# Performance work log

Hardware: AMD Instinct MI355X
Metric: run time of the kernel (lower is better)

Reference implementation:

```python
import jax, jax.numpy as jnp
import numpy as np

B, S, D, H, DH = 2, 2048, 256, 8, 32
INNER = H * DH


def setup_inputs() -> dict:
    key = jax.random.key(0)
    ks = jax.random.split(key, 8)
    x = jax.random.normal(ks[0], (B, S, D), dtype=jnp.float32)
    mask = jax.random.randint(ks[1], (B, S), 0, 2) > 0  # bool, ~half valid
    attn_bias = jax.random.normal(ks[2], (B, H, S, S), dtype=jnp.float32) * 0.1
    Wq = jax.random.normal(ks[3], (D, INNER), dtype=jnp.float32) * 0.02
    Wkv = jax.random.normal(ks[4], (D, 2 * INNER), dtype=jnp.float32) * 0.02
    Wo = jax.random.normal(ks[5], (INNER, D), dtype=jnp.float32) * 0.02
    bo = jnp.zeros((D,), dtype=jnp.float32)
    Wg = jax.random.normal(ks[6], (D, INNER), dtype=jnp.float32) * 0.02
    bg = jnp.ones((INNER,), dtype=jnp.float32)  # torch init: gating bias = 1.0
    return {"x": x, "mask": mask, "attn_bias": attn_bias, "Wq": Wq,
            "Wkv": Wkv, "Wo": Wo, "bo": bo, "Wg": Wg, "bg": bg}


def reference(x, mask, attn_bias, Wq, Wkv, Wo, bo, Wg, bg):
    scale = DH ** -0.5
    b, s, _ = x.shape
    # q,k,v projections; '... i (h d) -> ... h i d'
    q = (x @ Wq).reshape(b, s, H, DH).swapaxes(1, 2)            # [b,h,s,d]
    kv = x @ Wkv
    k, v = jnp.split(kv, 2, axis=-1)
    k = k.reshape(b, s, H, DH).swapaxes(1, 2)                   # [b,h,s,d]
    v = v.reshape(b, s, H, DH).swapaxes(1, 2)                   # [b,h,s,d]
    # scores with additive bias and boolean masking
    dots = jnp.einsum('bhid,bhjd->bhij', q * scale, k) + attn_bias
    amask = mask[:, None, :, None] & mask[:, None, None, :]     # [b,1,i,j]
    neg = -jnp.finfo(dots.dtype).max
    dots = jnp.where(amask, dots, neg)
    attn = jax.nn.softmax(dots, axis=-1)                        # dropout p=0 (eval)
    out = jnp.einsum('bhij,bhjd->bhid', attn, v)
    out = out.swapaxes(1, 2).reshape(b, s, INNER)               # '... h i d -> ... i (h d)'
    gates = jax.nn.sigmoid(x @ Wg + bg)
    out = out * gates
    return out @ Wo + bo
```

## Files before the change

### kernel.cpp

```cpp
#include <hip/hip_runtime.h>
#include <float.h>

typedef unsigned short u16;
typedef __attribute__((ext_vector_type(8))) short bf16x8;
typedef __attribute__((ext_vector_type(4))) float f32x4;

#define LOG2E 1.4426950408889634f
#define B_ 2
#define S_ 2048
#define D_ 256
#define H_ 8
#define DH_ 32
#define M_ 4096

__device__ __forceinline__ void gload_lds16(const void* g, void* l) {
  __builtin_amdgcn_global_load_lds(
      (const __attribute__((address_space(1))) unsigned int*)g,
      (__attribute__((address_space(3))) unsigned int*)l, 16, 0, 0);
}

__device__ __forceinline__ u16 f2bf(float f) {
  unsigned u = __float_as_uint(f);
  unsigned r = (u + 0x7FFFu + ((u >> 16) & 1u)) >> 16;
  return (u16)r;
}

__global__ __launch_bounds__(256) void conv_x(const float* __restrict__ x,
                                              u16* __restrict__ xb) {
  int i = (blockIdx.x * 256 + threadIdx.x) * 4;
  float4 v = *(const float4*)(x + i);
  ushort4 o;
  o.x = f2bf(v.x); o.y = f2bf(v.y); o.z = f2bf(v.z); o.w = f2bf(v.w);
  *(ushort4*)(xb + i) = o;
}

__global__ __launch_bounds__(256) void prep_w(const float* __restrict__ Wq,
                                              const float* __restrict__ Wkv,
                                              const float* __restrict__ Wo,
                                              const float* __restrict__ Wg,
                                              u16* __restrict__ wt,
                                              u16* __restrict__ wot) {
  int t = blockIdx.x * 256 + threadIdx.x;
  const float scale = 0.17677669529663687f;
  if (t < 65536) {
    int k = t >> 8, n = t & 255;
    wt[(size_t)n * 256 + k] = f2bf(Wq[t] * scale);
  } else if (t < 196608) {
    int s = t - 65536;
    int k = s >> 9, c = s & 511;
    int n = (c < 256) ? (256 + c) : (512 + (c - 256));
    wt[(size_t)n * 256 + k] = f2bf(Wkv[s]);
  } else if (t < 262144) {
    int s = t - 196608;
    int k = s >> 8, n = s & 255;
    wt[(size_t)(768 + n) * 256 + k] = f2bf(Wg[s]);
  } else {
    int s = t - 262144;
    int k = s >> 8, n = s & 255;
    wot[(size_t)n * 256 + k] = f2bf(Wo[s]);
  }
}

__global__ __launch_bounds__(64) void pack_mask(const int* __restrict__ mask,
                                                unsigned* __restrict__ cmT) {
  int b = blockIdx.x, c = threadIdx.x;
  unsigned wd = 0;
#pragma unroll
  for (int jc = 0; jc < 32; ++jc)
    wd |= (unsigned)(mask[b * 2048 + jc * 64 + c] & 1) << jc;
  cmT[b * 64 + c] = wd;
}

__global__ __launch_bounds__(256) void gemm_proj(
    const u16* __restrict__ xb, const u16* __restrict__ wt,
    const float* __restrict__ bg, u16* __restrict__ qs, u16* __restrict__ kb,
    u16* __restrict__ vt, float* __restrict__ gates) {
  __shared__ u16 lA[2][128 * 32];
  __shared__ u16 lB[2][128 * 32];
  const int tid = threadIdx.x, l = tid & 63, w = tid >> 6;
  const int m0 = blockIdx.x * 128, n0 = blockIdx.y * 128;
  const int wm = w >> 1, wn = w & 1;
  f32x4 acc[4][4];
#pragma unroll
  for (int i = 0; i < 4; ++i)
#pragma unroll
    for (int j = 0; j < 4; ++j) acc[i][j] = (f32x4){0.f, 0.f, 0.f, 0.f};

  auto stage = [&](int ks, int p) {
#pragma unroll
    for (int i = 0; i < 2; ++i) {
      int slot = i * 256 + tid;
      int row = slot >> 2, sk = slot & 3;
      int sw = sk ^ ((row >> 1) & 3);
      gload_lds16(xb + (size_t)(m0 + row) * 256 + ks * 32 + sw * 8,
                  (char*)lA[p] + slot * 16);
    }
#pragma unroll
    for (int i = 0; i < 2; ++i) {
      int slot = i * 256 + tid;
      int row = slot >> 2, sk = slot & 3;
      int sw = sk ^ ((row >> 1) & 3);
      gload_lds16(wt + (size_t)(n0 + row) * 256 + ks * 32 + sw * 8,
                  (char*)lB[p] + slot * 16);
    }
  };

  stage(0, 0);
  asm volatile("s_waitcnt vmcnt(0)" ::: "memory");
  __builtin_amdgcn_s_barrier();

  for (int ks = 0; ks < 8; ++ks) {
    const int cur = ks & 1;
    if (ks < 7) {
      stage(ks + 1, cur ^ 1);
      asm volatile("s_waitcnt vmcnt(4)" ::: "memory");
    } else {
      asm volatile("s_waitcnt vmcnt(0)" ::: "memory");
    }
    __builtin_amdgcn_s_barrier();

    bf16x8 af[4], bfr[4];
#pragma unroll
    for (int mi = 0; mi < 4; ++mi) {
      int row = wm * 64 + mi * 16 + (l & 15);
      int koff = ((l >> 4) << 4) ^ (((row >> 1) & 3) << 4);
      af[mi] = *(const bf16x8*)((const char*)lA[cur] + row * 64 + koff);
    }
#pragma unroll
    for (int ni = 0; ni < 4; ++ni) {
      int row = wn * 64 + ni * 16 + (l & 15);
      int koff = ((l >> 4) << 4) ^ (((row >> 1) & 3) << 4);
      bfr[ni] = *(const bf16x8*)((const char*)lB[cur] + row * 64 + koff);
    }
#pragma unroll
    for (int mi = 0; mi < 4; ++mi)
#pragma unroll
      for (int ni = 0; ni < 4; ++ni)
        acc[mi][ni] = __builtin_amdgcn_mfma_f32_16x16x32_bf16(
            af[mi], bfr[ni], acc[mi][ni], 0, 0, 0);
    __builtin_amdgcn_sched_barrier(0);
    __builtin_amdgcn_s_barrier();
  }
  const int region = n0 >> 8;
#pragma unroll
  for (int mi = 0; mi < 4; ++mi)
#pragma unroll
    for (int ni = 0; ni < 4; ++ni) {
      int row = m0 + wm * 64 + mi * 16 + ((l >> 4) << 2);
      int col = n0 + wn * 64 + ni * 16 + (l & 15);
      int c = col & 255;
#pragma unroll
      for (int r = 0; r < 4; ++r) {
        float v = acc[mi][ni][r];
        int rr = row + r;
        int bq = rr >> 11, s = rr & 2047;
        if (region == 0) {
          int h = c >> 5, dh = c & 31;
          qs[((((size_t)bq * 8 + h) * 2048 + s) << 5) + dh] = f2bf(v);
        } else if (region == 1) {
          int h = c >> 5, dh = c & 31;
          kb[((((size_t)bq * 8 + h) * 2048 + s) << 5) + dh] = f2bf(v);
        } else if (region == 2) {
          int h = c >> 5, dh = c & 31;
          vt[((((size_t)bq * 8 + h) * 32 + dh) << 11) + s] = f2bf(v);
        } else {
          float g = 1.f / (1.f + expf(-(v + bg[c])));
          gates[(size_t)rr * 256 + c] = g;
        }
      }
    }
}

__global__ __launch_bounds__(256) void attn_fwd(
    const u16* __restrict__ qs, const u16* __restrict__ kb,
    const u16* __restrict__ vt, const float* __restrict__ bias,
    const int* __restrict__ mask, const unsigned* __restrict__ cmT,
    const float* __restrict__ gates, u16* __restrict__ ao) {
  __shared__ u16 lK[2][64 * 32];
  __shared__ u16 lV[2][32 * 64];
  __shared__ float lBias[2][64 * 64];
  __shared__ u16 lP[4][16 * 64];
  const int tid = threadIdx.x, l = tid & 63, w = tid >> 6;
  const int qt = blockIdx.x, h = blockIdx.y, b = blockIdx.z;
  const int q0 = qt * 64;
  const size_t bh = (size_t)b * H_ + h;

  const int qrow = q0 + w * 16 + (l & 15);
  bf16x8 qf = *(const bf16x8*)(qs + ((bh * S_ + qrow) << 5) + ((l >> 4) << 3));

  int rowr[4], mi_[4];
  float m_i[4], l_i[4];
  unsigned cm[4];
  f32x4 acc_o[2];
  acc_o[0] = (f32x4){0.f, 0.f, 0.f, 0.f};
  acc_o[1] = (f32x4){0.f, 0.f, 0.f, 0.f};
#pragma unroll
  for (int r = 0; r < 4; ++r) {
    rowr[r] = q0 + w * 16 + ((l >> 4) << 2) + r;
    mi_[r] = mask[b * S_ + rowr[r]] & 1;
    m_i[r] = -FLT_MAX;
    l_i[r] = 0.f;
  }
#pragma unroll
  for (int cg = 0; cg < 4; ++cg) cm[cg] = cmT[(b << 6) + cg * 16 + (l & 15)];

  auto stage = [&](int jc, int p) {
    const int j0 = jc * 64;
    {
      int row = tid >> 2, sk = tid & 3;
      int sw = sk ^ ((row >> 1) & 3);
      gload_lds16(kb + ((bh * S_ + j0 + row) << 5) + sw * 8,
                  (char*)lK[p] + tid * 16);
    }
    {
      int dh = tid >> 3, sk = tid & 7;
      int sw = sk ^ (dh & 7);
      gload_lds16(vt + ((bh * 32 + dh) << 11) + j0 + sw * 8,
                  (char*)lV[p] + tid * 16);
    }
#pragma unroll
    for (int i = 0; i < 4; ++i) {
      int u = i * 256 + tid;
      int row = u >> 4, cb = u & 15;
      gload_lds16(bias + (bh * S_ + q0 + row) * (size_t)S_ + j0 + cb * 4,
                  (char*)lBias[p] + u * 16);
    }
  };

  stage(0, 0);
  asm volatile("s_waitcnt vmcnt(0)" ::: "memory");
  __builtin_amdgcn_s_barrier();

  for (int jc = 0; jc < 32; ++jc) {
    const int cur = jc & 1;
    if (jc < 31) {
      stage(jc + 1, cur ^ 1);
      asm volatile("s_waitcnt vmcnt(6)" ::: "memory");
    } else {
      asm volatile("s_waitcnt vmcnt(0)" ::: "memory");
    }
    __builtin_amdgcn_s_barrier();

    f32x4 sc[4];
#pragma unroll
    for (int cg = 0; cg < 4; ++cg) {
      int colj = cg * 16 + (l & 15);
      int mj = (int)((cm[cg] >> jc) & 1u);
      f32x4 ci;
#pragma unroll
      for (int r = 0; r < 4; ++r) {
        int qlr = w * 16 + ((l >> 4) << 2) + r;
        float bv = lBias[cur][qlr * 64 + colj];
        ci[r] = (mi_[r] & mj) ? bv : -FLT_MAX;
      }
      int krow = cg * 16 + (l & 15);
      int koff = ((l >> 4) << 4) ^ (((krow >> 1) & 3) << 4);
      bf16x8 kf = *(const bf16x8*)((const char*)lK[cur] + krow * 64 + koff);
      sc[cg] = __builtin_amdgcn_mfma_f32_16x16x32_bf16(qf, kf, ci, 0, 0, 0);
    }

    float corr[4];
#pragma unroll
    for (int r = 0; r < 4; ++r) {
      float v0 = fmaxf(fmaxf(sc[0][r], sc[1][r]), fmaxf(sc[2][r], sc[3][r]));
#pragma unroll
      for (int off = 1; off < 16; off <<= 1) v0 = fmaxf(v0, __shfl_xor(v0, off));
      float mn = fmaxf(m_i[r], v0);
      corr[r] = exp2f((m_i[r] - mn) * LOG2E);
      m_i[r] = mn;
    }
    float rs[4] = {0.f, 0.f, 0.f, 0.f};
#pragma unroll
    for (int cg = 0; cg < 4; ++cg) {
#pragma unroll
      for (int r = 0; r < 4; ++r) {
        float p = exp2f((sc[cg][r] - m_i[r]) * LOG2E);
        rs[r] += p;
        int prow = ((l >> 4) << 2) + r;
        int col = cg * 16 + (l & 15);
        *(u16*)((char*)lP[w] + prow * 128 + ((col * 2) ^ ((prow & 7) << 4))) =
            f2bf(p);
      }
    }
#pragma unroll
    for (int r = 0; r < 4; ++r) {
      float s = rs[r];
#pragma unroll
      for (int off = 1; off < 16; off <<= 1) s += __shfl_xor(s, off);
      l_i[r] = l_i[r] * corr[r] + s;
    }
#pragma unroll
    for (int g = 0; g < 2; ++g)
#pragma unroll
      for (int r = 0; r < 4; ++r) acc_o[g][r] *= corr[r];

#pragma unroll
    for (int kp = 0; kp < 2; ++kp) {
      int prow = l & 15;
      int koff = (((l >> 4) << 4) + kp * 64) ^ ((prow & 7) << 4);
      bf16x8 pf = *(const bf16x8*)((const char*)lP[w] + prow * 128 + koff);
#pragma unroll
      for (int g = 0; g < 2; ++g) {
        int vrow = g * 16 + (l & 15);
        int vkoff = (((l >> 4) << 4) + kp * 64) ^ ((vrow & 7) << 4);
        bf16x8 vf = *(const bf16x8*)((const char*)lV[cur] + vrow * 128 + vkoff);
        acc_o[g] = __builtin_amdgcn_mfma_f32_16x16x32_bf16(pf, vf, acc_o[g], 0, 0, 0);
      }
    }
    __builtin_amdgcn_sched_barrier(0);
    __builtin_amdgcn_s_barrier();
  }

#pragma unroll
  for (int g = 0; g < 2; ++g)
#pragma unroll
    for (int r = 0; r < 4; ++r) {
      int rr = rowr[r];
      int dh = g * 16 + (l & 15);
      float gate = gates[(size_t)(b * S_ + rr) * 256 + h * 32 + dh];
      float o = acc_o[g][r] / l_i[r] * gate;
      ao[(size_t)(b * S_ + rr) * 256 + h * 32 + dh] = f2bf(o);
    }
}

__global__ __launch_bounds__(256) void gemm_out(const u16* __restrict__ ao,
                                                const u16* __restrict__ wot,
                                                const float* __restrict__ bo,
                                                float* __restrict__ out) {
  __shared__ u16 lA[128 * 32];
  __shared__ u16 lB[128 * 32];
  const int tid = threadIdx.x, l = tid & 63, w = tid >> 6;
  const int m0 = blockIdx.x * 128, n0 = blockIdx.y * 128;
  const int wm = w >> 1, wn = w & 1;
  f32x4 acc[4][4];
#pragma unroll
  for (int i = 0; i < 4; ++i)
#pragma unroll
    for (int j = 0; j < 4; ++j) acc[i][j] = (f32x4){0.f, 0.f, 0.f, 0.f};

  for (int ks = 0; ks < 8; ++ks) {
#pragma unroll
    for (int i = 0; i < 2; ++i) {
      int slot = i * 256 + tid;
      int row = slot >> 2, sk = slot & 3;
      int sw = sk ^ ((row >> 1) & 3);
      gload_lds16(ao + (size_t)(m0 + row) * 256 + ks * 32 + sw * 8,
                  (char*)lA + slot * 16);
    }
#pragma unroll
    for (int i = 0; i < 2; ++i) {
      int slot = i * 256 + tid;
      int row = slot >> 2, sk = slot & 3;
      int sw = sk ^ ((row >> 1) & 3);
      gload_lds16(wot + (size_t)(n0 + row) * 256 + ks * 32 + sw * 8,
                  (char*)lB + slot * 16);
    }
    __syncthreads();
    bf16x8 af[4], bfr[4];
#pragma unroll
    for (int mi = 0; mi < 4; ++mi) {
      int row = wm * 64 + mi * 16 + (l & 15);
      int koff = ((l >> 4) << 4) ^ (((row >> 1) & 3) << 4);
      af[mi] = *(const bf16x8*)((const char*)lA + row * 64 + koff);
    }
#pragma unroll
    for (int ni = 0; ni < 4; ++ni) {
      int row = wn * 64 + ni * 16 + (l & 15);
      int koff = ((l >> 4) << 4) ^ (((row >> 1) & 3) << 4);
      bfr[ni] = *(const bf16x8*)((const char*)lB + row * 64 + koff);
    }
#pragma unroll
    for (int mi = 0; mi < 4; ++mi)
#pragma unroll
      for (int ni = 0; ni < 4; ++ni)
        acc[mi][ni] = __builtin_amdgcn_mfma_f32_16x16x32_bf16(
            af[mi], bfr[ni], acc[mi][ni], 0, 0, 0);
    __syncthreads();
  }
#pragma unroll
  for (int mi = 0; mi < 4; ++mi)
#pragma unroll
    for (int ni = 0; ni < 4; ++ni) {
      int row = m0 + wm * 64 + mi * 16 + ((l >> 4) << 2);
      int col = n0 + wn * 64 + ni * 16 + (l & 15);
#pragma unroll
      for (int r = 0; r < 4; ++r)
        out[(size_t)(row + r) * 256 + col] = acc[mi][ni][r] + bo[col];
    }
}

extern "C" void kernel_launch(void* const* d_in, const int* in_sizes, int n_in,
                              void* d_out, int out_size, void* d_ws,
                              size_t ws_size, hipStream_t stream) {
  const float* x   = (const float*)d_in[0];
  const int* mask  = (const int*)d_in[1];
  const float* bias = (const float*)d_in[2];
  const float* Wq  = (const float*)d_in[3];
  const float* Wkv = (const float*)d_in[4];
  const float* Wo  = (const float*)d_in[5];
  const float* bo  = (const float*)d_in[6];
  const float* Wg  = (const float*)d_in[7];
  const float* bg  = (const float*)d_in[8];

  char* ws = (char*)d_ws;
  u16* xb      = (u16*)(ws);
  u16* wt      = (u16*)(ws + 2097152);
  u16* wot     = (u16*)(ws + 2621440);
  u16* qs      = (u16*)(ws + 2752512);
  u16* kb      = (u16*)(ws + 4849664);
  u16* vt      = (u16*)(ws + 6946816);
  float* gates = (float*)(ws + 9043968);
  u16* ao      = (u16*)(ws + 13238272);
  unsigned* cmT = (unsigned*)(ws + 15335424);
  float* out   = (float*)d_out;

  conv_x<<<dim3(1024), dim3(256), 0, stream>>>(x, xb);
  prep_w<<<dim3(1280), dim3(256), 0, stream>>>(Wq, Wkv, Wo, Wg, wt, wot);
  pack_mask<<<dim3(2), dim3(64), 0, stream>>>(mask, cmT);
  gemm_proj<<<dim3(32, 8), dim3(256), 0, stream>>>(xb, wt, bg, qs, kb, vt, gates);
  attn_fwd<<<dim3(32, 8, 2), dim3(256), 0, stream>>>(qs, kb, vt, bias, mask, cmT, gates, ao);
  gemm_out<<<dim3(32, 2), dim3(256), 0, stream>>>(ao, wot, bo, out);
}
```

Before: 438.6 us.

## Single-buffer bias tile in attention, restage after QK, merge prep kernels

Three prep kernels (x conversion, weight transpose, mask packing) are merged into one launch to cut launch overhead. In the attention kernel the bias tile goes from double to single buffer, halving the largest LDS allocation. The next tile's K/V/bias loads now issue after the QK MFMAs have read the current bias, with launch_bounds(256,4) set to raise occupancy. The trade-off is less prefetch overlap, since the loop now waits for all outstanding loads at the end of every iteration.

```diff
diff --git a/kernel.cpp b/kernel.cpp
--- a/kernel.cpp
+++ b/kernel.cpp
@@ -25,50 +25,49 @@
   return (u16)r;
 }
 
-__global__ __launch_bounds__(256) void conv_x(const float* __restrict__ x,
-                                              u16* __restrict__ xb) {
-  int i = (blockIdx.x * 256 + threadIdx.x) * 4;
-  float4 v = *(const float4*)(x + i);
-  ushort4 o;
-  o.x = f2bf(v.x); o.y = f2bf(v.y); o.z = f2bf(v.z); o.w = f2bf(v.w);
-  *(ushort4*)(xb + i) = o;
-}
-
-__global__ __launch_bounds__(256) void prep_w(const float* __restrict__ Wq,
-                                              const float* __restrict__ Wkv,
-                                              const float* __restrict__ Wo,
-                                              const float* __restrict__ Wg,
-                                              u16* __restrict__ wt,
-                                              u16* __restrict__ wot) {
-  int t = blockIdx.x * 256 + threadIdx.x;
-  const float scale = 0.17677669529663687f;
-  if (t < 65536) {
-    int k = t >> 8, n = t & 255;
-    wt[(size_t)n * 256 + k] = f2bf(Wq[t] * scale);
-  } else if (t < 196608) {
-    int s = t - 65536;
-    int k = s >> 9, c = s & 511;
-    int n = (c < 256) ? (256 + c) : (512 + (c - 256));
-    wt[(size_t)n * 256 + k] = f2bf(Wkv[s]);
-  } else if (t < 262144) {
-    int s = t - 196608;
-    int k = s >> 8, n = s & 255;
-    wt[(size_t)(768 + n) * 256 + k] = f2bf(Wg[s]);
+__global__ __launch_bounds__(256) void prep_all(
+    const float* __restrict__ x, const float* __restrict__ Wq,
+    const float* __restrict__ Wkv, const float* __restrict__ Wo,
+    const float* __restrict__ Wg, const int* __restrict__ mask,
+    u16* __restrict__ xb, u16* __restrict__ wt, u16* __restrict__ wot,
+    unsigned* __restrict__ cmT) {
+  const int bi = blockIdx.x, tid = threadIdx.x;
+  if (bi < 1024) {
+    int i = (bi * 256 + tid) * 4;
+    float4 v = *(const float4*)(x + i);
+    ushort4 o;
+    o.x = f2bf(v.x); o.y = f2bf(v.y); o.z = f2bf(v.z); o.w = f2bf(v.w);
+    *(ushort4*)(xb + i) = o;
+  } else if (bi < 2304) {
+    int t = (bi - 1024) * 256 + tid;
+    const float scale = 0.17677669529663687f;
+    if (t < 65536) {
+      int k = t >> 8, n = t & 255;
+      wt[(size_t)n * 256 + k] = f2bf(Wq[t] * scale);
+    } else if (t < 196608) {
+      int s = t - 65536;
+      int k = s >> 9, c = s & 511;
+      int n = (c < 256) ? (256 + c) : (512 + (c - 256));
+      wt[(size_t)n * 256 + k] = f2bf(Wkv[s]);
+    } else if (t < 262144) {
+      int s = t - 196608;
+      int k = s >> 8, n = s & 255;
+      wt[(size_t)(768 + n) * 256 + k] = f2bf(Wg[s]);
+    } else {
+      int s = t - 262144;
+      int k = s >> 8, n = s & 255;
+      wot[(size_t)n * 256 + k] = f2bf(Wo[s]);
+    }
   } else {
-    int s = t - 262144;
-    int k = s >> 8, n = s & 255;
-    wot[(size_t)n * 256 + k] = f2bf(Wo[s]);
+    if (tid < 128) {
+      int b = tid >> 6, c = tid & 63;
+      unsigned wd = 0;
+#pragma unroll
+      for (int jc = 0; jc < 32; ++jc)
+        wd |= (unsigned)(mask[b * 2048 + jc * 64 + c] & 1) << jc;
+      cmT[b * 64 + c] = wd;
+    }
   }
-}
-
-__global__ __launch_bounds__(64) void pack_mask(const int* __restrict__ mask,
-                                                unsigned* __restrict__ cmT) {
-  int b = blockIdx.x, c = threadIdx.x;
-  unsigned wd = 0;
-#pragma unroll
-  for (int jc = 0; jc < 32; ++jc)
-    wd |= (unsigned)(mask[b * 2048 + jc * 64 + c] & 1) << jc;
-  cmT[b * 64 + c] = wd;
 }
 
 __global__ __launch_bounds__(256) void gemm_proj(
@@ -171,14 +170,14 @@
     }
 }
 
-__global__ __launch_bounds__(256) void attn_fwd(
+__global__ __launch_bounds__(256, 4) void attn_fwd(
     const u16* __restrict__ qs, const u16* __restrict__ kb,
     const u16* __restrict__ vt, const float* __restrict__ bias,
     const int* __restrict__ mask, const unsigned* __restrict__ cmT,
     const float* __restrict__ gates, u16* __restrict__ ao) {
   __shared__ u16 lK[2][64 * 32];
   __shared__ u16 lV[2][32 * 64];
-  __shared__ float lBias[2][64 * 64];
+  __shared__ float lBias[64 * 64];
   __shared__ u16 lP[4][16 * 64];
   const int tid = threadIdx.x, l = tid & 63, w = tid >> 6;
   const int qt = blockIdx.x, h = blockIdx.y, b = blockIdx.z;
@@ -204,7 +203,7 @@
 #pragma unroll
   for (int cg = 0; cg < 4; ++cg) cm[cg] = cmT[(b << 6) + cg * 16 + (l & 15)];
 
-  auto stage = [&](int jc, int p) {
+  auto stageKV = [&](int jc, int p) {
     const int j0 = jc * 64;
     {
       int row = tid >> 2, sk = tid & 3;
@@ -218,28 +217,25 @@
       gload_lds16(vt + ((bh * 32 + dh) << 11) + j0 + sw * 8,
                   (char*)lV[p] + tid * 16);
     }
+  };
+  auto stageBias = [&](int jc) {
+    const int j0 = jc * 64;
 #pragma unroll
     for (int i = 0; i < 4; ++i) {
-      int u = i * 256 + tid;
-      int row = u >> 4, cb = u & 15;
+      int u = i * 64 + l;
+      int row = w * 16 + (u >> 4), cb = u & 15;
       gload_lds16(bias + (bh * S_ + q0 + row) * (size_t)S_ + j0 + cb * 4,
-                  (char*)lBias[p] + u * 16);
+                  (char*)lBias + (w * 256 + u) * 16);
     }
   };
 
-  stage(0, 0);
+  stageKV(0, 0);
+  stageBias(0);
   asm volatile("s_waitcnt vmcnt(0)" ::: "memory");
   __builtin_amdgcn_s_barrier();
 
   for (int jc = 0; jc < 32; ++jc) {
     const int cur = jc & 1;
-    if (jc < 31) {
-      stage(jc + 1, cur ^ 1);
-      asm volatile("s_waitcnt vmcnt(6)" ::: "memory");
-    } else {
-      asm volatile("s_waitcnt vmcnt(0)" ::: "memory");
-    }
-    __builtin_amdgcn_s_barrier();
 
     f32x4 sc[4];
 #pragma unroll
@@ -250,13 +246,20 @@
 #pragma unroll
       for (int r = 0; r < 4; ++r) {
         int qlr = w * 16 + ((l >> 4) << 2) + r;
-        float bv = lBias[cur][qlr * 64 + colj];
+        float bv = lBias[qlr * 64 + colj];
         ci[r] = (mi_[r] & mj) ? bv : -FLT_MAX;
       }
       int krow = cg * 16 + (l & 15);
       int koff = ((l >> 4) << 4) ^ (((krow >> 1) & 3) << 4);
       bf16x8 kf = *(const bf16x8*)((const char*)lK[cur] + krow * 64 + koff);
       sc[cg] = __builtin_amdgcn_mfma_f32_16x16x32_bf16(qf, kf, ci, 0, 0, 0);
+    }
+
+    asm volatile("s_waitcnt lgkmcnt(0)" ::: "memory");
+    __builtin_amdgcn_sched_barrier(0);
+    if (jc < 31) {
+      stageKV(jc + 1, cur ^ 1);
+      stageBias(jc + 1);
     }
 
     float corr[4];
@@ -308,6 +311,7 @@
       }
     }
     __builtin_amdgcn_sched_barrier(0);
+    asm volatile("s_waitcnt vmcnt(0)" ::: "memory");
     __builtin_amdgcn_s_barrier();
   }
 
@@ -414,9 +418,8 @@
   unsigned* cmT = (unsigned*)(ws + 15335424);
   float* out   = (float*)d_out;
 
-  conv_x<<<dim3(1024), dim3(256), 0, stream>>>(x, xb);
-  prep_w<<<dim3(1280), dim3(256), 0, stream>>>(Wq, Wkv, Wo, Wg, wt, wot);
-  pack_mask<<<dim3(2), dim3(64), 0, stream>>>(mask, cmT);
+  prep_all<<<dim3(2305), dim3(256), 0, stream>>>(x, Wq, Wkv, Wo, Wg, mask,
+                                                 xb, wt, wot, cmT);
   gemm_proj<<<dim3(32, 8), dim3(256), 0, stream>>>(xb, wt, bg, qs, kb, vt, gates);
   attn_fwd<<<dim3(32, 8, 2), dim3(256), 0, stream>>>(qs, kb, vt, bias, mask, cmT, gates, ao);
   gemm_out<<<dim3(32, 2), dim3(256), 0, stream>>>(ao, wot, bo, out);
```

Measured after the change: 434.0 us. About the same (-1.1%).
